# Kernel optimization log

Hardware: AMD Instinct MI355X
Metric: run time of the kernel (lower is better)

Reference implementation:

```python
import jax, jax.numpy as jnp
import numpy as np

B, T, C, H = 2, 2048, 1024, 16

def setup_inputs() -> dict:
    key = jax.random.key(0)
    k1, k2, k3 = jax.random.split(key, 3)
    scale = 0.02
    return {
        "x": jax.random.normal(k1, (B, T, C), dtype=jnp.float32),
        "w_attn": jax.random.normal(k2, (C, 3 * C), dtype=jnp.float32) * scale,
        "b_attn": jnp.zeros((3 * C,), dtype=jnp.float32),
        "w_proj": jax.random.normal(k3, (C, C), dtype=jnp.float32) * scale,
        "b_proj": jnp.zeros((C,), dtype=jnp.float32),
    }

def reference(x, w_attn, b_attn, w_proj, b_proj):
    Bx, Tx, Cx = x.shape
    hd = Cx // H  # head dim
    qkv = x @ w_attn + b_attn  # [B,T,3C]
    q, k, v = jnp.split(qkv, 3, axis=-1)
    # [B,H,T,hd]
    q = q.reshape(Bx, Tx, H, hd).transpose(0, 2, 1, 3)
    k = k.reshape(Bx, Tx, H, hd).transpose(0, 2, 1, 3)
    v = v.reshape(Bx, Tx, H, hd).transpose(0, 2, 1, 3)
    att = jnp.einsum('bhqd,bhkd->bhqk', q, k) * (1.0 / jnp.sqrt(jnp.float32(hd)))
    causal = jnp.tril(jnp.ones((Tx, Tx), dtype=bool))  # [T,T]
    att = jnp.where(causal[None, None], att, jnp.float32(-jnp.inf))
    att = jax.nn.softmax(att, axis=-1)
    y = jnp.einsum('bhqk,bhkd->bhqd', att, v)  # [B,H,T,hd]
    y = y.transpose(0, 2, 1, 3).reshape(Bx, Tx, Cx)
    return y @ w_proj + b_proj
```

## Files before the change

### kernel.cpp

```cpp
#include <hip/hip_runtime.h>
#include <hip/hip_bf16.h>
#include <stdint.h>

#define B_SZ 2
#define T_SZ 2048
#define C_SZ 1024
#define H_SZ 16
#define HD   64
#define BH   (B_SZ * H_SZ)
#define M_SZ (B_SZ * T_SZ)
#define N_QKV (3 * C_SZ)

typedef __attribute__((ext_vector_type(8))) __bf16 bf16x8;
typedef __attribute__((ext_vector_type(4))) float f32x4;
typedef __attribute__((ext_vector_type(8))) unsigned short us8;
typedef __attribute__((ext_vector_type(4))) unsigned short us4;
typedef __attribute__((ext_vector_type(4))) unsigned int u32x4;

__device__ __forceinline__ unsigned short f2bf(float f) {
    unsigned int u = __builtin_bit_cast(unsigned int, f);
    u += 0x7fffu + ((u >> 16) & 1u);
    return (unsigned short)(u >> 16);
}

__device__ __forceinline__ void gll16(const unsigned short* g, unsigned short* l) {
    __builtin_amdgcn_global_load_lds(
        (const __attribute__((address_space(1))) unsigned int*)g,
        (__attribute__((address_space(3))) unsigned int*)l, 16, 0, 0);
}

__device__ __forceinline__ void hard_sync() {
    asm volatile("s_waitcnt vmcnt(0) lgkmcnt(0)" ::: "memory");
    __builtin_amdgcn_sched_barrier(0);
    __syncthreads();
}

__global__ __launch_bounds__(256) void k_prep(const float* __restrict__ x,
                                              const float* __restrict__ wa,
                                              const float* __restrict__ wp,
                                              unsigned short* __restrict__ xb,
                                              unsigned short* __restrict__ wta,
                                              unsigned short* __restrict__ wtp) {
    __shared__ float tile[32][33];
    const int tid = threadIdx.x;
    int idx = blockIdx.x;
    if (idx < 2048) {
        const size_t i = ((size_t)idx * 256 + tid) * 8;
        f32x4 a = *(const f32x4*)(x + i);
        f32x4 b = *(const f32x4*)(x + i + 4);
        us8 o;
        #pragma unroll
        for (int j = 0; j < 4; ++j) { o[j] = f2bf(a[j]); o[4 + j] = f2bf(b[j]); }
        *(us8*)(xb + i) = o;
        return;
    }
    const float* in; unsigned short* out; int N;
    if (idx < 5120) { idx -= 2048; in = wa; out = wta; N = N_QKV; }
    else            { idx -= 5120; in = wp; out = wtp; N = C_SZ; }
    const int nx = N / 32;
    const int n0 = (idx % nx) * 32, k0 = (idx / nx) * 32;
    const int tx = tid & 31, ty = tid >> 5;
    #pragma unroll
    for (int j = 0; j < 32; j += 8)
        tile[ty + j][tx] = in[(size_t)(k0 + ty + j) * N + (n0 + tx)];
    __syncthreads();
    #pragma unroll
    for (int j = 0; j < 32; j += 8)
        out[(size_t)(n0 + ty + j) * C_SZ + (k0 + tx)] = f2bf(tile[tx][ty + j]);
}

template <int EPI>
__global__ __launch_bounds__(256) void k_gemm(const unsigned short* __restrict__ A,
                                              const unsigned short* __restrict__ Bt,
                                              const float* __restrict__ bias,
                                              float* __restrict__ Cout,
                                              unsigned short* __restrict__ q_ws,
                                              unsigned short* __restrict__ k_ws,
                                              unsigned short* __restrict__ vT_ws,
                                              int M, int N, int K, int NX) {
    __shared__ __attribute__((aligned(16))) unsigned short Ald[128 * 64];
    __shared__ __attribute__((aligned(16))) unsigned short Bld[128 * 64];
    const int tid = threadIdx.x;
    const int wid = tid >> 6, lane = tid & 63;
    const int wr = wid >> 1, wc = wid & 1;
    const int g = lane >> 4, l15 = lane & 15;
    const int nwg = gridDim.x;
    const int wg = (blockIdx.x & 7) * (nwg >> 3) + (blockIdx.x >> 3);
    const int m0 = (wg / NX) * 128, n0 = (wg % NX) * 128;

    f32x4 acc[4][4];
    #pragma unroll
    for (int i = 0; i < 4; ++i)
        #pragma unroll
        for (int j = 0; j < 4; ++j) acc[i][j] = (f32x4){0.f, 0.f, 0.f, 0.f};

    for (int k0 = 0; k0 < K; k0 += 64) {
        hard_sync();
        #pragma unroll
        for (int i = 0; i < 4; ++i) {
            int c = i * 256 + tid;
            int row = c >> 3;
            int colb = ((c & 7) << 4) ^ ((row & 7) << 4);
            gll16(A  + (size_t)(m0 + row) * K + k0 + (colb >> 1), Ald + i * 2048 + wid * 512);
            gll16(Bt + (size_t)(n0 + row) * K + k0 + (colb >> 1), Bld + i * 2048 + wid * 512);
        }
        hard_sync();

        #pragma unroll
        for (int ks = 0; ks < 2; ++ks) {
            bf16x8 af[4], bfr[4];
            #pragma unroll
            for (int mi = 0; mi < 4; ++mi) {
                int row = wr * 64 + mi * 16 + l15;
                af[mi] = *(const bf16x8*)((const char*)Ald + row * 128 +
                                          ((ks * 64 + g * 16) ^ ((row & 7) << 4)));
            }
            #pragma unroll
            for (int nj = 0; nj < 4; ++nj) {
                int row = wc * 64 + nj * 16 + l15;
                bfr[nj] = *(const bf16x8*)((const char*)Bld + row * 128 +
                                           ((ks * 64 + g * 16) ^ ((row & 7) << 4)));
            }
            #pragma unroll
            for (int mi = 0; mi < 4; ++mi)
                #pragma unroll
                for (int nj = 0; nj < 4; ++nj)
                    acc[mi][nj] = __builtin_amdgcn_mfma_f32_16x16x32_bf16(
                        af[mi], bfr[nj], acc[mi][nj], 0, 0, 0);
        }
    }

    if (EPI == 0) {
        #pragma unroll
        for (int nj = 0; nj < 4; ++nj) {
            int col = n0 + wc * 64 + nj * 16 + l15;
            float bv = bias[col];
            #pragma unroll
            for (int mi = 0; mi < 4; ++mi) {
                int rowb = m0 + wr * 64 + mi * 16 + g * 4;
                #pragma unroll
                for (int r = 0; r < 4; ++r)
                    Cout[(size_t)(rowb + r) * N + col] = acc[mi][nj][r] + bv;
            }
        }
    } else {
        #pragma unroll
        for (int nj = 0; nj < 4; ++nj) {
            int col = n0 + wc * 64 + nj * 16 + l15;
            float bv = bias[col];
            int which = col >> 10;
            int c10 = col & 1023;
            int h = c10 >> 6, d = c10 & 63;
            #pragma unroll
            for (int mi = 0; mi < 4; ++mi) {
                #pragma unroll
                for (int r = 0; r < 4; ++r) {
                    int row = m0 + wr * 64 + mi * 16 + g * 4 + r;
                    int bb = row >> 11, t = row & 2047;
                    unsigned short val = f2bf(acc[mi][nj][r] + bv);
                    if (which == 2)
                        vT_ws[((size_t)(bb * H_SZ + h) * HD + d) * T_SZ + t] = val;
                    else
                        (which ? k_ws : q_ws)[((size_t)(bb * H_SZ + h) * T_SZ + t) * HD + d] = val;
                }
            }
        }
    }
}

__global__ __launch_bounds__(256) void k_attn(const unsigned short* __restrict__ q_ws,
                                              const unsigned short* __restrict__ k_ws,
                                              const unsigned short* __restrict__ vT_ws,
                                              unsigned short* __restrict__ y_ws) {
    __shared__ __attribute__((aligned(16))) unsigned short Kbuf[2][8192];
    __shared__ __attribute__((aligned(16))) unsigned short Vbuf[2][8192];
    const int tid = threadIdx.x;
    const int wid = tid >> 6, lane = tid & 63;
    const int g = lane >> 4, l15 = lane & 15;
    const int n = blockIdx.x;
    const int xcd = n & 7, j = (n >> 3) & 15, rk = n >> 7;
    const int bh = xcd + 8 * rk;
    const size_t kv_off = (size_t)bh * T_SZ * HD;
    const unsigned short* Kg = k_ws + kv_off;
    const unsigned short* Vg = vT_ws + (size_t)bh * HD * T_SZ;
    const int b = bh >> 4, h = bh & 15;
    const float SC = 0.125f * 1.44269504f;
    const int qloc = wid * 16 + l15;

    auto stageK = [&](int kv, int buf) {
        #pragma unroll
        for (int i = 0; i < 4; ++i) {
            int c = i * 256 + tid;
            int row = c >> 3;
            int colb = ((c & 7) << 4) ^ ((row & 7) << 4);
            gll16(Kg + (size_t)(kv * 128 + row) * HD + (colb >> 1),
                  &Kbuf[buf][i * 2048 + wid * 512]);
        }
    };
    auto stageV = [&](int kv, int buf) {
        #pragma unroll
        for (int i = 0; i < 4; ++i) {
            int c = i * 256 + tid;
            int row = c >> 4;
            int colb = ((c & 15) << 4) ^ ((row & 15) << 4);
            gll16(Vg + (size_t)row * T_SZ + kv * 128 + (colb >> 1),
                  &Vbuf[buf][i * 2048 + wid * 512]);
        }
    };

    #pragma unroll 1
    for (int phase = 0; phase < 2; ++phase) {
        const int qb = phase ? j : (31 - j);
        const int nkv = (qb + 2) >> 1;

        const int qrow = qb * 64 + wid * 16 + l15;
        bf16x8 aq[2];
        aq[0] = *(const bf16x8*)(q_ws + kv_off + (size_t)qrow * HD + g * 8);
        aq[1] = *(const bf16x8*)(q_ws + kv_off + (size_t)qrow * HD + 32 + g * 8);

        float m_run = -3e38f, l_run = 0.f;
        f32x4 acc[4];
        #pragma unroll
        for (int dt = 0; dt < 4; ++dt) acc[dt] = (f32x4){0.f, 0.f, 0.f, 0.f};

        hard_sync();
        stageK(0, 0); stageV(0, 0);
        int cur = 0;

        for (int kv = 0; kv < nkv; ++kv) {
            hard_sync();
            if (kv + 1 < nkv) { stageK(kv + 1, cur ^ 1); stageV(kv + 1, cur ^ 1); }
            const char* Kb = (const char*)Kbuf[cur];
            const char* Vb = (const char*)Vbuf[cur];

            f32x4 st[8];
            __builtin_amdgcn_s_setprio(1);
            #pragma unroll
            for (int kt = 0; kt < 8; ++kt) {
                f32x4 sv = (f32x4){0.f, 0.f, 0.f, 0.f};
                #pragma unroll
                for (int ks = 0; ks < 2; ++ks) {
                    int row = kt * 16 + l15;
                    bf16x8 ak = *(const bf16x8*)(Kb + row * 128 +
                                                 ((ks * 64 + g * 16) ^ ((row & 7) << 4)));
                    sv = __builtin_amdgcn_mfma_f32_16x16x32_bf16(ak, aq[ks], sv, 0, 0, 0);
                }
                st[kt] = sv;
            }
            __builtin_amdgcn_s_setprio(0);

            float t[32];
            #pragma unroll
            for (int kt = 0; kt < 8; ++kt)
                #pragma unroll
                for (int r = 0; r < 4; ++r) t[kt * 4 + r] = st[kt][r];
            if (kv == nkv - 1) {
                const int off = kv * 128 - qb * 64;
                #pragma unroll
                for (int kt = 0; kt < 8; ++kt)
                    #pragma unroll
                    for (int r = 0; r < 4; ++r)
                        if (kt * 16 + g * 4 + r + off > qloc) t[kt * 4 + r] = -3e38f;
            }

            float m16[16];
            #pragma unroll
            for (int i = 0; i < 16; ++i) m16[i] = fmaxf(t[i], t[i + 16]);
            float m8[8];
            #pragma unroll
            for (int i = 0; i < 8; ++i) m8[i] = fmaxf(m16[i], m16[i + 8]);
            float m4[4];
            #pragma unroll
            for (int i = 0; i < 4; ++i) m4[i] = fmaxf(m8[i], m8[i + 4]);
            float mx = fmaxf(fmaxf(m4[0], m4[1]), fmaxf(m4[2], m4[3]));
            mx = fmaxf(mx, __shfl_xor(mx, 16, 64));
            mx = fmaxf(mx, __shfl_xor(mx, 32, 64));
            float mt = mx * SC;

            if (!__all(mt - m_run <= 8.0f)) {
                float mnew = fmaxf(m_run, mt);
                float alpha = exp2f(m_run - mnew);
                m_run = mnew;
                l_run *= alpha;
                float ao[4];
                #pragma unroll
                for (int r = 0; r < 4; ++r) {
                    int ai = __builtin_amdgcn_ds_bpermute((g * 4 + r) * 4,
                                                          __builtin_bit_cast(int, alpha));
                    ao[r] = __builtin_bit_cast(float, ai);
                }
                #pragma unroll
                for (int dt = 0; dt < 4; ++dt)
                    #pragma unroll
                    for (int r = 0; r < 4; ++r) acc[dt][r] *= ao[r];
            }

            float p[32];
            #pragma unroll
            for (int i = 0; i < 32; ++i) p[i] = exp2f(fmaf(t[i], SC, -m_run));
            float s16[16];
            #pragma unroll
            for (int i = 0; i < 16; ++i) s16[i] = p[i] + p[i + 16];
            float s8[8];
            #pragma unroll
            for (int i = 0; i < 8; ++i) s8[i] = s16[i] + s16[i + 8];
            float s4[4];
            #pragma unroll
            for (int i = 0; i < 4; ++i) s4[i] = s8[i] + s8[i + 4];
            float sum = (s4[0] + s4[1]) + (s4[2] + s4[3]);
            sum += __shfl_xor(sum, 16, 64);
            sum += __shfl_xor(sum, 32, 64);
            l_run += sum;

            unsigned int pk0[8], pk1[8];
            #pragma unroll
            for (int kt = 0; kt < 8; ++kt) {
                asm("v_cvt_pk_bf16_f32 %0, %1, %2" : "=v"(pk0[kt]) : "v"(p[kt * 4 + 0]), "v"(p[kt * 4 + 1]));
                asm("v_cvt_pk_bf16_f32 %0, %1, %2" : "=v"(pk1[kt]) : "v"(p[kt * 4 + 2]), "v"(p[kt * 4 + 3]));
            }
            __builtin_amdgcn_s_setprio(1);
            #pragma unroll
            for (int ks = 0; ks < 4; ++ks) {
                unsigned int x0 = pk0[2 * ks], y0 = pk0[2 * ks + 1];
                unsigned int x1 = pk1[2 * ks], y1 = pk1[2 * ks + 1];
                asm("v_permlane32_swap_b32 %0, %1" : "+v"(x0), "+v"(y0));
                asm("v_permlane16_swap_b32 %0, %1" : "+v"(x0), "+v"(y0));
                asm("v_permlane32_swap_b32 %0, %1" : "+v"(x1), "+v"(y1));
                asm("v_permlane16_swap_b32 %0, %1" : "+v"(x1), "+v"(y1));
                bf16x8 ap = __builtin_bit_cast(bf16x8, (u32x4){x0, x1, y0, y1});
                #pragma unroll
                for (int dt = 0; dt < 4; ++dt) {
                    int row = dt * 16 + l15;
                    bf16x8 bv = *(const bf16x8*)(Vb + row * 256 +
                                                 ((ks * 64 + g * 16) ^ ((row & 15) << 4)));
                    acc[dt] = __builtin_amdgcn_mfma_f32_16x16x32_bf16(ap, bv, acc[dt], 0, 0, 0);
                }
            }
            __builtin_amdgcn_s_setprio(0);
            cur ^= 1;
        }

        float lo[4];
        #pragma unroll
        for (int r = 0; r < 4; ++r) {
            int li = __builtin_amdgcn_ds_bpermute((g * 4 + r) * 4,
                                                  __builtin_bit_cast(int, l_run));
            lo[r] = __builtin_bit_cast(float, li);
        }
        #pragma unroll
        for (int r = 0; r < 4; ++r) {
            int tq = qb * 64 + wid * 16 + g * 4 + r;
            float inv = 1.0f / lo[r];
            #pragma unroll
            for (int dt = 0; dt < 4; ++dt)
                y_ws[(size_t)(b * T_SZ + tq) * C_SZ + h * 64 + dt * 16 + l15] =
                    f2bf(acc[dt][r] * inv);
        }
    }
}

extern "C" void kernel_launch(void* const* d_in, const int* in_sizes, int n_in,
                              void* d_out, int out_size, void* d_ws, size_t ws_size,
                              hipStream_t stream) {
    const float* x      = (const float*)d_in[0];
    const float* w_attn = (const float*)d_in[1];
    const float* b_attn = (const float*)d_in[2];
    const float* w_proj = (const float*)d_in[3];
    const float* b_proj = (const float*)d_in[4];
    float* out = (float*)d_out;

    char* ws = (char*)d_ws;
    unsigned short* q_ws  = (unsigned short*)(ws + 0);
    unsigned short* k_ws  = (unsigned short*)(ws + 8388608);
    unsigned short* vT_ws = (unsigned short*)(ws + 16777216);
    unsigned short* wtp   = (unsigned short*)(ws + 25165824);
    unsigned short* xb    = (unsigned short*)(ws + 27262976);
    unsigned short* y_ws  = (unsigned short*)(ws + 27262976);
    unsigned short* wta   = (unsigned short*)(ws + 35651584);

    k_prep<<<dim3(6144), 256, 0, stream>>>(x, w_attn, w_proj, xb, wta, wtp);

    k_gemm<1><<<dim3((N_QKV / 128) * (M_SZ / 128)), 256, 0, stream>>>(
        xb, wta, b_attn, nullptr, q_ws, k_ws, vT_ws, M_SZ, N_QKV, C_SZ, N_QKV / 128);

    k_attn<<<dim3(512), 256, 0, stream>>>(q_ws, k_ws, vT_ws, y_ws);

    k_gemm<0><<<dim3((C_SZ / 128) * (M_SZ / 128)), 256, 0, stream>>>(
        y_ws, wtp, b_proj, out, nullptr, nullptr, nullptr, M_SZ, C_SZ, C_SZ, C_SZ / 128);
}
```

Baseline: 119.0 us.

## Enlarge attention query tile to 128 rows with 8-wave blocks sharing K/V staging

The attention kernel now runs 256 blocks of 512 threads. Each block handles a 128-row query tile with 8 waves instead of a 64-row tile with 4 waves, so every staged K/V tile in shared memory is reused by twice as many query rows and global K/V traffic is halved. The causal mask now only applies to the diagonal tile, and the row-sum cross-lane shuffle moves out of the kv loop into the epilogue. In exchange there are half as many blocks, which may reduce occupancy and load balance across CUs.

```diff
diff --git a/kernel.cpp b/kernel.cpp
--- a/kernel.cpp
+++ b/kernel.cpp
@@ -168,7 +168,7 @@
     }
 }
 
-__global__ __launch_bounds__(256) void k_attn(const unsigned short* __restrict__ q_ws,
+__global__ __launch_bounds__(512) void k_attn(const unsigned short* __restrict__ q_ws,
                                               const unsigned short* __restrict__ k_ws,
                                               const unsigned short* __restrict__ vT_ws,
                                               unsigned short* __restrict__ y_ws) {
@@ -178,7 +178,7 @@
     const int wid = tid >> 6, lane = tid & 63;
     const int g = lane >> 4, l15 = lane & 15;
     const int n = blockIdx.x;
-    const int xcd = n & 7, j = (n >> 3) & 15, rk = n >> 7;
+    const int xcd = n & 7, j = (n >> 3) & 7, rk = n >> 6;
     const int bh = xcd + 8 * rk;
     const size_t kv_off = (size_t)bh * T_SZ * HD;
     const unsigned short* Kg = k_ws + kv_off;
@@ -189,36 +189,36 @@
 
     auto stageK = [&](int kv, int buf) {
         #pragma unroll
-        for (int i = 0; i < 4; ++i) {
-            int c = i * 256 + tid;
+        for (int i = 0; i < 2; ++i) {
+            int c = i * 512 + tid;
             int row = c >> 3;
             int colb = ((c & 7) << 4) ^ ((row & 7) << 4);
             gll16(Kg + (size_t)(kv * 128 + row) * HD + (colb >> 1),
-                  &Kbuf[buf][i * 2048 + wid * 512]);
+                  &Kbuf[buf][i * 4096 + wid * 512]);
         }
     };
     auto stageV = [&](int kv, int buf) {
         #pragma unroll
-        for (int i = 0; i < 4; ++i) {
-            int c = i * 256 + tid;
+        for (int i = 0; i < 2; ++i) {
+            int c = i * 512 + tid;
             int row = c >> 4;
             int colb = ((c & 15) << 4) ^ ((row & 15) << 4);
             gll16(Vg + (size_t)row * T_SZ + kv * 128 + (colb >> 1),
-                  &Vbuf[buf][i * 2048 + wid * 512]);
+                  &Vbuf[buf][i * 4096 + wid * 512]);
         }
     };
 
     #pragma unroll 1
     for (int phase = 0; phase < 2; ++phase) {
-        const int qb = phase ? j : (31 - j);
-        const int nkv = (qb + 2) >> 1;
-
-        const int qrow = qb * 64 + wid * 16 + l15;
+        const int qt = phase ? j : (15 - j);
+        const int nkv = qt + 1;
+
+        const int qrow = qt * 128 + wid * 16 + l15;
         bf16x8 aq[2];
         aq[0] = *(const bf16x8*)(q_ws + kv_off + (size_t)qrow * HD + g * 8);
         aq[1] = *(const bf16x8*)(q_ws + kv_off + (size_t)qrow * HD + 32 + g * 8);
 
-        float m_run = -3e38f, l_run = 0.f;
+        float m_run = -3e38f, l_part = 0.f;
         f32x4 acc[4];
         #pragma unroll
         for (int dt = 0; dt < 4; ++dt) acc[dt] = (f32x4){0.f, 0.f, 0.f, 0.f};
@@ -255,24 +255,24 @@
                 #pragma unroll
                 for (int r = 0; r < 4; ++r) t[kt * 4 + r] = st[kt][r];
             if (kv == nkv - 1) {
-                const int off = kv * 128 - qb * 64;
+                const int ql = wid * 16 + l15;
                 #pragma unroll
                 for (int kt = 0; kt < 8; ++kt)
                     #pragma unroll
                     for (int r = 0; r < 4; ++r)
-                        if (kt * 16 + g * 4 + r + off > qloc) t[kt * 4 + r] = -3e38f;
+                        if (kt * 16 + g * 4 + r > ql) t[kt * 4 + r] = -3e38f;
             }
 
             float m16[16];
             #pragma unroll
             for (int i = 0; i < 16; ++i) m16[i] = fmaxf(t[i], t[i + 16]);
-            float m8[8];
-            #pragma unroll
-            for (int i = 0; i < 8; ++i) m8[i] = fmaxf(m16[i], m16[i + 8]);
-            float m4[4];
-            #pragma unroll
-            for (int i = 0; i < 4; ++i) m4[i] = fmaxf(m8[i], m8[i + 4]);
-            float mx = fmaxf(fmaxf(m4[0], m4[1]), fmaxf(m4[2], m4[3]));
+            float m8v[8];
+            #pragma unroll
+            for (int i = 0; i < 8; ++i) m8v[i] = fmaxf(m16[i], m16[i + 8]);
+            float m4v[4];
+            #pragma unroll
+            for (int i = 0; i < 4; ++i) m4v[i] = fmaxf(m8v[i], m8v[i + 4]);
+            float mx = fmaxf(fmaxf(m4v[0], m4v[1]), fmaxf(m4v[2], m4v[3]));
             mx = fmaxf(mx, __shfl_xor(mx, 16, 64));
             mx = fmaxf(mx, __shfl_xor(mx, 32, 64));
             float mt = mx * SC;
@@ -281,7 +281,7 @@
                 float mnew = fmaxf(m_run, mt);
                 float alpha = exp2f(m_run - mnew);
                 m_run = mnew;
-                l_run *= alpha;
+                l_part *= alpha;
                 float ao[4];
                 #pragma unroll
                 for (int r = 0; r < 4; ++r) {
@@ -301,16 +301,13 @@
             float s16[16];
             #pragma unroll
             for (int i = 0; i < 16; ++i) s16[i] = p[i] + p[i + 16];
-            float s8[8];
-            #pragma unroll
-            for (int i = 0; i < 8; ++i) s8[i] = s16[i] + s16[i + 8];
-            float s4[4];
-            #pragma unroll
-            for (int i = 0; i < 4; ++i) s4[i] = s8[i] + s8[i + 4];
-            float sum = (s4[0] + s4[1]) + (s4[2] + s4[3]);
-            sum += __shfl_xor(sum, 16, 64);
-            sum += __shfl_xor(sum, 32, 64);
-            l_run += sum;
+            float s8v[8];
+            #pragma unroll
+            for (int i = 0; i < 8; ++i) s8v[i] = s16[i] + s16[i + 8];
+            float s4v[4];
+            #pragma unroll
+            for (int i = 0; i < 4; ++i) s4v[i] = s8v[i] + s8v[i + 4];
+            l_part += (s4v[0] + s4v[1]) + (s4v[2] + s4v[3]);
 
             unsigned int pk0[8], pk1[8];
             #pragma unroll
@@ -340,16 +337,19 @@
             cur ^= 1;
         }
 
+        float lsum = l_part;
+        lsum += __shfl_xor(lsum, 16, 64);
+        lsum += __shfl_xor(lsum, 32, 64);
         float lo[4];
         #pragma unroll
         for (int r = 0; r < 4; ++r) {
             int li = __builtin_amdgcn_ds_bpermute((g * 4 + r) * 4,
-                                                  __builtin_bit_cast(int, l_run));
+                                                  __builtin_bit_cast(int, lsum));
             lo[r] = __builtin_bit_cast(float, li);
         }
         #pragma unroll
         for (int r = 0; r < 4; ++r) {
-            int tq = qb * 64 + wid * 16 + g * 4 + r;
+            int tq = qt * 128 + wid * 16 + g * 4 + r;
             float inv = 1.0f / lo[r];
             #pragma unroll
             for (int dt = 0; dt < 4; ++dt)
@@ -383,7 +383,7 @@
     k_gemm<1><<<dim3((N_QKV / 128) * (M_SZ / 128)), 256, 0, stream>>>(
         xb, wta, b_attn, nullptr, q_ws, k_ws, vT_ws, M_SZ, N_QKV, C_SZ, N_QKV / 128);
 
-    k_attn<<<dim3(512), 256, 0, stream>>>(q_ws, k_ws, vT_ws, y_ws);
+    k_attn<<<dim3(256), 512, 0, stream>>>(q_ws, k_ws, vT_ws, y_ws);
 
     k_gemm<0><<<dim3((C_SZ / 128) * (M_SZ / 128)), 256, 0, stream>>>(
         y_ws, wtp, b_proj, out, nullptr, nullptr, nullptr, M_SZ, C_SZ, C_SZ, C_SZ / 128);
```

Result: no change. 118.1 us (-0.8%).
